# Performance work log

Measured on AMD Instinct MI355X. Metric: run time of the kernel, lower is better.

## Reference

```python
import jax, jax.numpy as jnp
import numpy as np

ND = 64       # dijetFeatures (channels)
NPAIR = 6     # six dijet slots


def _interleave(x, d):
    # x: [n, nd, 12] -> [n, nd, 6, 2]; d: [n, nd, 6] -> [n, nd, 6, 1]
    n, nd, _ = x.shape
    xr = x.reshape(n, nd, NPAIR, 2)
    z = jnp.concatenate([xr, d[..., None]], axis=-1)  # [n, nd, 6, 3]
    return z


def _conv_s3(z, W, b):
    # z: [n, in, 6, 3] grouped windows; W: [out, in, 3]; stride-3 k-3 conv == per-window contraction
    return jnp.einsum('bisk,oik->bos', z, W) + b[None, :, None]  # [n, out, 6]


def setup_inputs() -> dict:
    key = jax.random.key(0)
    ks = jax.random.split(key, 8)
    n = 65536
    inp = {
        'x': jax.random.normal(ks[0], (n, ND, 12), dtype=jnp.float32),
        'd': jax.random.normal(ks[1], (n, ND, NPAIR), dtype=jnp.float32),
        'W1': jax.random.normal(ks[2], (ND, ND, 3), dtype=jnp.float32) * 0.05,
        'b1': jax.random.normal(ks[3], (ND,), dtype=jnp.float32) * 0.05,
        'W2': jax.random.normal(ks[4], (ND, ND, 3), dtype=jnp.float32) * 0.05,
        'b2': jax.random.normal(ks[5], (ND,), dtype=jnp.float32) * 0.05,
        'W3': jax.random.normal(ks[6], (ND, ND, 3), dtype=jnp.float32) * 0.05,
        'b3': jax.random.normal(ks[7], (ND,), dtype=jnp.float32) * 0.05,
    }
    return inp


def reference(x, d, W1, b1, W2, b2, W3, b3):
    d1 = d
    d = jax.nn.relu(_conv_s3(_interleave(x, d), W1, b1))
    d = jax.nn.relu(_conv_s3(_interleave(x, d), W2, b2))
    d = _conv_s3(_interleave(x, d), W3, b3)
    return jax.nn.relu(d + d1)
```

## Files before the change

### kernel.cpp

```cpp
#include <hip/hip_runtime.h>

#define ND 64
#define NPAIR 6

typedef short bf16x8 __attribute__((ext_vector_type(8)));
typedef float floatx4 __attribute__((ext_vector_type(4)));

static constexpr int SPB  = 8;
static constexpr int ROWS = SPB * NPAIR;
static constexpr int ASTR = 200;

__device__ __forceinline__ unsigned short f2bf(float f) {
    unsigned u = __builtin_bit_cast(unsigned, f);
    u += 0x7FFFu + ((u >> 16) & 1u);
    return (unsigned short)(u >> 16);
}
__device__ __forceinline__ unsigned f2bf2(float lo, float hi) {
    return (unsigned)f2bf(lo) | ((unsigned)f2bf(hi) << 16);
}

__global__ void repack_w(const float* __restrict__ W1, const float* __restrict__ W2,
                         const float* __restrict__ W3, unsigned short* __restrict__ P) {
    int idx = blockIdx.x * 256 + threadIdx.x;
    if (idx >= 3 * 64 * 192) return;
    int j = idx % 192;
    int n = (idx / 192) % 64;
    int L = idx / (192 * 64);
    const float* W = (L == 0) ? W1 : (L == 1) ? W2 : W3;
    float v = (j < 128) ? W[n * 192 + (j >> 1) * 3 + (j & 1)]
                        : W[n * 192 + (j - 128) * 3 + 2];
    P[idx] = f2bf(v);
}

__global__ __launch_bounds__(256, 7) void dijet_main(
    const float* __restrict__ x, const float* __restrict__ d,
    const float* __restrict__ b1, const float* __restrict__ b2,
    const float* __restrict__ b3, const unsigned short* __restrict__ Wp,
    float* __restrict__ out)
{
    __shared__ __align__(16) unsigned short A[ROWS * ASTR];
    float* Ct = (float*)A;

    const int t  = threadIdx.x;
    const int b0 = blockIdx.x * SPB;

    float2 dres[6];
    {
        const float2* d2 = (const float2*)(d + (size_t)b0 * (ND * NPAIR));
        #pragma unroll
        for (int m = 0; m < 6; ++m) dres[m] = d2[m * 256 + t];
    }
    {
        const float4* x4 = (const float4*)(x + (size_t)b0 * (ND * 12));
        float4 v[6];
        #pragma unroll
        for (int m = 0; m < 6; ++m) v[m] = x4[m * 256 + t];
        unsigned* A32 = (unsigned*)A;
        #pragma unroll
        for (int m = 0; m < 6; ++m) {
            int idx = m * 256 + t;
            int b   = idx / 192;
            int rem = idx - b * 192;
            int i   = rem / 3;
            int c0  = (rem - i * 3) * 4;
            int row0 = b * 6 + (c0 >> 1);
            A32[row0 * (ASTR / 2) + i]       = f2bf2(v[m].x, v[m].y);
            A32[(row0 + 1) * (ASTR / 2) + i] = f2bf2(v[m].z, v[m].w);
        }
    }
    {
        #pragma unroll
        for (int m = 0; m < 6; ++m) {
            int idx = m * 256 + t;
            int e   = idx * 2;
            int b   = e / 384;
            int rem = e - b * 384;
            int i   = rem / 6;
            int s   = rem - i * 6;
            int row = b * 6 + s;
            A[row * ASTR + 128 + i]       = f2bf(dres[m].x);
            A[(row + 1) * ASTR + 128 + i] = f2bf(dres[m].y);
        }
    }
    __syncthreads();

    const int wave = t >> 6;
    const int lane = t & 63;
    const int l15  = lane & 15;
    const int quad = lane >> 4;
    const int nbase = wave * 16;

    #pragma unroll
    for (int L = 0; L < 3; ++L) {
        const float* bL = (L == 0) ? b1 : (L == 1) ? b2 : b3;
        const unsigned short* WL = Wp + L * (64 * 192);

        bf16x8 Bf[6];
        #pragma unroll
        for (int kk = 0; kk < 6; ++kk)
            Bf[kk] = *(const bf16x8*)(WL + (nbase + l15) * 192 + kk * 32 + quad * 8);
        float bias = bL[nbase + l15];

        floatx4 acc[3] = {};
        #pragma unroll
        for (int kk = 0; kk < 6; ++kk) {
            #pragma unroll
            for (int mt = 0; mt < 3; ++mt) {
                bf16x8 Af = *(const bf16x8*)(A + (mt * 16 + l15) * ASTR + kk * 32 + quad * 8);
                acc[mt] = __builtin_amdgcn_mfma_f32_16x16x32_bf16(Af, Bf[kk], acc[mt], 0, 0, 0);
            }
        }

        const int o = nbase + l15;
        if (L < 2) {
            __syncthreads();
            #pragma unroll
            for (int mt = 0; mt < 3; ++mt) {
                #pragma unroll
                for (int r = 0; r < 4; ++r) {
                    int row = mt * 16 + quad * 4 + r;
                    float v = acc[mt][r] + bias;
                    v = v > 0.f ? v : 0.f;
                    A[row * ASTR + 128 + o] = f2bf(v);
                }
            }
            __syncthreads();
        } else {
            __syncthreads();
            #pragma unroll
            for (int mt = 0; mt < 3; ++mt) {
                #pragma unroll
                for (int r = 0; r < 4; ++r) {
                    int row = mt * 16 + quad * 4 + r;
                    int bl  = row / 6;
                    int s   = row - bl * 6;
                    Ct[bl * (ND * NPAIR) + o * NPAIR + s] = acc[mt][r] + bias;
                }
            }
            __syncthreads();
            float2* out2 = (float2*)(out + (size_t)b0 * (ND * NPAIR));
            const float2* Ct2 = (const float2*)Ct;
            #pragma unroll
            for (int m = 0; m < 6; ++m) {
                int idx = m * 256 + t;
                float2 c = Ct2[idx];
                float2 r;
                r.x = c.x + dres[m].x; r.x = r.x > 0.f ? r.x : 0.f;
                r.y = c.y + dres[m].y; r.y = r.y > 0.f ? r.y : 0.f;
                out2[idx] = r;
            }
        }
    }
}

extern "C" void kernel_launch(void* const* d_in, const int* in_sizes, int n_in,
                              void* d_out, int out_size, void* d_ws, size_t ws_size,
                              hipStream_t stream)
{
    const float* x  = (const float*)d_in[0];
    const float* dd = (const float*)d_in[1];
    const float* W1 = (const float*)d_in[2];
    const float* b1 = (const float*)d_in[3];
    const float* W2 = (const float*)d_in[4];
    const float* b2 = (const float*)d_in[5];
    const float* W3 = (const float*)d_in[6];
    const float* b3 = (const float*)d_in[7];
    float* out = (float*)d_out;
    unsigned short* Wp = (unsigned short*)d_ws;

    int n = in_sizes[0] / (ND * 12);

    repack_w<<<144, 256, 0, stream>>>(W1, W2, W3, Wp);
    dijet_main<<<n / SPB, 256, 0, stream>>>(x, dd, b1, b2, b3, Wp, out);
}
```

Baseline: 392.5 us.

## Give each wave its own row tile and keep x fragments in registers

The work split changes from four waves each owning 16 output channels across all 48 rows to three waves each owning 16 rows across all 64 channels. The x part of the A operand is converted to bf16 straight into registers and reused across all three layers. Only the d/activation part goes through a smaller per-wave LDS region, so the block-wide barriers between layers go away and the layer outputs can be written as packed stores. The cost is that weight fragments are now read from global memory (L1/L2) inside the MFMA chain, x is loaded with strided float2 reads, and the block shrinks to 192 threads with a separate Ct buffer.

```diff
diff --git a/kernel.cpp b/kernel.cpp
--- a/kernel.cpp
+++ b/kernel.cpp
@@ -8,7 +8,7 @@
 
 static constexpr int SPB  = 8;
 static constexpr int ROWS = SPB * NPAIR;
-static constexpr int ASTR = 200;
+static constexpr int DSTR = 72;
 
 __device__ __forceinline__ unsigned short f2bf(float f) {
     unsigned u = __builtin_bit_cast(unsigned, f);
@@ -32,122 +32,115 @@
     P[idx] = f2bf(v);
 }
 
-__global__ __launch_bounds__(256, 7) void dijet_main(
+__global__ __launch_bounds__(192, 4) void dijet_main(
     const float* __restrict__ x, const float* __restrict__ d,
     const float* __restrict__ b1, const float* __restrict__ b2,
     const float* __restrict__ b3, const unsigned short* __restrict__ Wp,
     float* __restrict__ out)
 {
-    __shared__ __align__(16) unsigned short A[ROWS * ASTR];
-    float* Ct = (float*)A;
+    __shared__ __align__(16) unsigned short Adp[ROWS * DSTR];
+    __shared__ __align__(16) float Ct[SPB * ND * NPAIR];
 
-    const int t  = threadIdx.x;
-    const int b0 = blockIdx.x * SPB;
+    const int t    = threadIdx.x;
+    const int b0   = blockIdx.x * SPB;
+    const int wv   = t >> 6;
+    const int lane = t & 63;
+    const int l15  = lane & 15;
+    const int quad = lane >> 4;
 
-    float2 dres[6];
+    float2 dres[SPB];
     {
         const float2* d2 = (const float2*)(d + (size_t)b0 * (ND * NPAIR));
         #pragma unroll
-        for (int m = 0; m < 6; ++m) dres[m] = d2[m * 256 + t];
-    }
-    {
-        const float4* x4 = (const float4*)(x + (size_t)b0 * (ND * 12));
-        float4 v[6];
+        for (int m = 0; m < SPB; ++m) dres[m] = d2[m * 192 + t];
+        const int di  = t / 3;
+        const int dsl = 2 * (t - 3 * (t / 3));
         #pragma unroll
-        for (int m = 0; m < 6; ++m) v[m] = x4[m * 256 + t];
-        unsigned* A32 = (unsigned*)A;
-        #pragma unroll
-        for (int m = 0; m < 6; ++m) {
-            int idx = m * 256 + t;
-            int b   = idx / 192;
-            int rem = idx - b * 192;
-            int i   = rem / 3;
-            int c0  = (rem - i * 3) * 4;
-            int row0 = b * 6 + (c0 >> 1);
-            A32[row0 * (ASTR / 2) + i]       = f2bf2(v[m].x, v[m].y);
-            A32[(row0 + 1) * (ASTR / 2) + i] = f2bf2(v[m].z, v[m].w);
+        for (int m = 0; m < SPB; ++m) {
+            Adp[(m * 6 + dsl)     * DSTR + di] = f2bf(dres[m].x);
+            Adp[(m * 6 + dsl + 1) * DSTR + di] = f2bf(dres[m].y);
         }
     }
+
+    const int row = 16 * wv + l15;
+    const int bs  = row / 6;
+    const int ss  = row - 6 * bs;
+    bf16x8 Ax[4];
     {
+        const float* xb = x + (size_t)(b0 + bs) * (ND * 12) + 2 * ss;
         #pragma unroll
-        for (int m = 0; m < 6; ++m) {
-            int idx = m * 256 + t;
-            int e   = idx * 2;
-            int b   = e / 384;
-            int rem = e - b * 384;
-            int i   = rem / 6;
-            int s   = rem - i * 6;
-            int row = b * 6 + s;
-            A[row * ASTR + 128 + i]       = f2bf(dres[m].x);
-            A[(row + 1) * ASTR + 128 + i] = f2bf(dres[m].y);
+        for (int kk = 0; kk < 4; ++kk) {
+            union { bf16x8 h; unsigned u[4]; } tmp;
+            #pragma unroll
+            for (int w = 0; w < 4; ++w) {
+                const float2 v = *(const float2*)(xb + (kk * 16 + quad * 4 + w) * 12);
+                tmp.u[w] = f2bf2(v.x, v.y);
+            }
+            Ax[kk] = tmp.h;
         }
     }
     __syncthreads();
 
-    const int wave = t >> 6;
-    const int lane = t & 63;
-    const int l15  = lane & 15;
-    const int quad = lane >> 4;
-    const int nbase = wave * 16;
+    const unsigned short* Arow = Adp + (16 * wv + l15) * DSTR + quad * 8;
 
     #pragma unroll
     for (int L = 0; L < 3; ++L) {
         const float* bL = (L == 0) ? b1 : (L == 1) ? b2 : b3;
-        const unsigned short* WL = Wp + L * (64 * 192);
+        const unsigned short* WL = Wp + L * (64 * 192) + quad * 8;
 
-        bf16x8 Bf[6];
+        const bf16x8 Ad0 = *(const bf16x8*)(Arow);
+        const bf16x8 Ad1 = *(const bf16x8*)(Arow + 32);
+
+        float bias[4];
+        floatx4 acc[4];
         #pragma unroll
-        for (int kk = 0; kk < 6; ++kk)
-            Bf[kk] = *(const bf16x8*)(WL + (nbase + l15) * 192 + kk * 32 + quad * 8);
-        float bias = bL[nbase + l15];
-
-        floatx4 acc[3] = {};
-        #pragma unroll
-        for (int kk = 0; kk < 6; ++kk) {
-            #pragma unroll
-            for (int mt = 0; mt < 3; ++mt) {
-                bf16x8 Af = *(const bf16x8*)(A + (mt * 16 + l15) * ASTR + kk * 32 + quad * 8);
-                acc[mt] = __builtin_amdgcn_mfma_f32_16x16x32_bf16(Af, Bf[kk], acc[mt], 0, 0, 0);
-            }
+        for (int nt = 0; nt < 4; ++nt) {
+            const int ch = 4 * l15 + nt;
+            const unsigned short* wr = WL + ch * 192;
+            bias[nt] = bL[ch];
+            floatx4 a = {0.f, 0.f, 0.f, 0.f};
+            a = __builtin_amdgcn_mfma_f32_16x16x32_bf16(Ax[0], *(const bf16x8*)(wr),       a, 0, 0, 0);
+            a = __builtin_amdgcn_mfma_f32_16x16x32_bf16(Ax[1], *(const bf16x8*)(wr + 32),  a, 0, 0, 0);
+            a = __builtin_amdgcn_mfma_f32_16x16x32_bf16(Ax[2], *(const bf16x8*)(wr + 64),  a, 0, 0, 0);
+            a = __builtin_amdgcn_mfma_f32_16x16x32_bf16(Ax[3], *(const bf16x8*)(wr + 96),  a, 0, 0, 0);
+            a = __builtin_amdgcn_mfma_f32_16x16x32_bf16(Ad0,   *(const bf16x8*)(wr + 128), a, 0, 0, 0);
+            a = __builtin_amdgcn_mfma_f32_16x16x32_bf16(Ad1,   *(const bf16x8*)(wr + 160), a, 0, 0, 0);
+            acc[nt] = a;
         }
 
-        const int o = nbase + l15;
         if (L < 2) {
-            __syncthreads();
             #pragma unroll
-            for (int mt = 0; mt < 3; ++mt) {
+            for (int r = 0; r < 4; ++r) {
+                float v0 = acc[0][r] + bias[0]; v0 = v0 > 0.f ? v0 : 0.f;
+                float v1 = acc[1][r] + bias[1]; v1 = v1 > 0.f ? v1 : 0.f;
+                float v2 = acc[2][r] + bias[2]; v2 = v2 > 0.f ? v2 : 0.f;
+                float v3 = acc[3][r] + bias[3]; v3 = v3 > 0.f ? v3 : 0.f;
+                uint2 pk;
+                pk.x = f2bf2(v0, v1);
+                pk.y = f2bf2(v2, v3);
+                *(uint2*)(Adp + (16 * wv + quad * 4 + r) * DSTR + 4 * l15) = pk;
+            }
+        } else {
+            #pragma unroll
+            for (int nt = 0; nt < 4; ++nt) {
                 #pragma unroll
                 for (int r = 0; r < 4; ++r) {
-                    int row = mt * 16 + quad * 4 + r;
-                    float v = acc[mt][r] + bias;
-                    v = v > 0.f ? v : 0.f;
-                    A[row * ASTR + 128 + o] = f2bf(v);
-                }
-            }
-            __syncthreads();
-        } else {
-            __syncthreads();
-            #pragma unroll
-            for (int mt = 0; mt < 3; ++mt) {
-                #pragma unroll
-                for (int r = 0; r < 4; ++r) {
-                    int row = mt * 16 + quad * 4 + r;
-                    int bl  = row / 6;
-                    int s   = row - bl * 6;
-                    Ct[bl * (ND * NPAIR) + o * NPAIR + s] = acc[mt][r] + bias;
+                    const int rw = 16 * wv + quad * 4 + r;
+                    const int bl = rw / 6;
+                    const int s  = rw - 6 * bl;
+                    Ct[bl * (ND * NPAIR) + (4 * l15 + nt) * NPAIR + s] = acc[nt][r] + bias[nt];
                 }
             }
             __syncthreads();
             float2* out2 = (float2*)(out + (size_t)b0 * (ND * NPAIR));
             const float2* Ct2 = (const float2*)Ct;
             #pragma unroll
-            for (int m = 0; m < 6; ++m) {
-                int idx = m * 256 + t;
-                float2 c = Ct2[idx];
-                float2 r;
-                r.x = c.x + dres[m].x; r.x = r.x > 0.f ? r.x : 0.f;
-                r.y = c.y + dres[m].y; r.y = r.y > 0.f ? r.y : 0.f;
-                out2[idx] = r;
+            for (int m = 0; m < SPB; ++m) {
+                float2 c = Ct2[m * 192 + t];
+                float2 rv;
+                rv.x = c.x + dres[m].x; rv.x = rv.x > 0.f ? rv.x : 0.f;
+                rv.y = c.y + dres[m].y; rv.y = rv.y > 0.f ? rv.y : 0.f;
+                out2[m * 192 + t] = rv;
             }
         }
     }
@@ -171,5 +164,5 @@
     int n = in_sizes[0] / (ND * 12);
 
     repack_w<<<144, 256, 0, stream>>>(W1, W2, W3, Wp);
-    dijet_main<<<n / SPB, 256, 0, stream>>>(x, dd, b1, b2, b3, Wp, out);
+    dijet_main<<<n / SPB, 192, 0, stream>>>(x, dd, b1, b2, b3, Wp, out);
 }
```

Result: slower. 523.6 us (+33.4%).

## Split LDS into swizzled x buffer and double-buffered d tiles, drop a barrier

Applied to the files above, without the earlier changes.

Replaces the padded single A tile (stride 200) with an unpadded x tile plus two ping-pong d tiles, using XOR swizzles so the MFMA operand reads avoid bank conflicts without padding. Double-buffering the d activations removes one __syncthreads per layer, since the next layer's input is written to the other buffer. The launch-bounds occupancy hint drops from 7 to 6, and the LDS footprint changes slightly.

```diff
diff --git a/kernel.cpp b/kernel.cpp
--- a/kernel.cpp
+++ b/kernel.cpp
@@ -8,7 +8,6 @@
 
 static constexpr int SPB  = 8;
 static constexpr int ROWS = SPB * NPAIR;
-static constexpr int ASTR = 200;
 
 __device__ __forceinline__ unsigned short f2bf(float f) {
     unsigned u = __builtin_bit_cast(unsigned, f);
@@ -18,6 +17,9 @@
 __device__ __forceinline__ unsigned f2bf2(float lo, float hi) {
     return (unsigned)f2bf(lo) | ((unsigned)f2bf(hi) << 16);
 }
+
+__device__ __forceinline__ int swzAx(int row, int c) { return (c & 8) | ((c ^ row) & 7); }
+__device__ __forceinline__ int swzD (int row, int c) { return (c ^ row) & 7; }
 
 __global__ void repack_w(const float* __restrict__ W1, const float* __restrict__ W2,
                          const float* __restrict__ W3, unsigned short* __restrict__ P) {
@@ -32,14 +34,15 @@
     P[idx] = f2bf(v);
 }
 
-__global__ __launch_bounds__(256, 7) void dijet_main(
+__global__ __launch_bounds__(256, 6) void dijet_main(
     const float* __restrict__ x, const float* __restrict__ d,
     const float* __restrict__ b1, const float* __restrict__ b2,
     const float* __restrict__ b3, const unsigned short* __restrict__ Wp,
     float* __restrict__ out)
 {
-    __shared__ __align__(16) unsigned short A[ROWS * ASTR];
-    float* Ct = (float*)A;
+    __shared__ __align__(16) unsigned short Ax[ROWS * 128];
+    __shared__ __align__(16) unsigned short Dd[2][ROWS * 64];
+    float* Ct = (float*)Ax;
 
     const int t  = threadIdx.x;
     const int b0 = blockIdx.x * SPB;
@@ -49,26 +52,6 @@
         const float2* d2 = (const float2*)(d + (size_t)b0 * (ND * NPAIR));
         #pragma unroll
         for (int m = 0; m < 6; ++m) dres[m] = d2[m * 256 + t];
-    }
-    {
-        const float4* x4 = (const float4*)(x + (size_t)b0 * (ND * 12));
-        float4 v[6];
-        #pragma unroll
-        for (int m = 0; m < 6; ++m) v[m] = x4[m * 256 + t];
-        unsigned* A32 = (unsigned*)A;
-        #pragma unroll
-        for (int m = 0; m < 6; ++m) {
-            int idx = m * 256 + t;
-            int b   = idx / 192;
-            int rem = idx - b * 192;
-            int i   = rem / 3;
-            int c0  = (rem - i * 3) * 4;
-            int row0 = b * 6 + (c0 >> 1);
-            A32[row0 * (ASTR / 2) + i]       = f2bf2(v[m].x, v[m].y);
-            A32[(row0 + 1) * (ASTR / 2) + i] = f2bf2(v[m].z, v[m].w);
-        }
-    }
-    {
         #pragma unroll
         for (int m = 0; m < 6; ++m) {
             int idx = m * 256 + t;
@@ -78,8 +61,28 @@
             int i   = rem / 6;
             int s   = rem - i * 6;
             int row = b * 6 + s;
-            A[row * ASTR + 128 + i]       = f2bf(dres[m].x);
-            A[(row + 1) * ASTR + 128 + i] = f2bf(dres[m].y);
+            Dd[0][row * 64       + swzD(row, i >> 3) * 8     + (i & 7)] = f2bf(dres[m].x);
+            Dd[0][(row + 1) * 64 + swzD(row + 1, i >> 3) * 8 + (i & 7)] = f2bf(dres[m].y);
+        }
+    }
+    {
+        const float4* x4 = (const float4*)(x + (size_t)b0 * (ND * 12));
+        float4 v[6];
+        #pragma unroll
+        for (int m = 0; m < 6; ++m) v[m] = x4[m * 256 + t];
+        unsigned* Ax32 = (unsigned*)Ax;
+        #pragma unroll
+        for (int m = 0; m < 6; ++m) {
+            int idx = m * 256 + t;
+            int b   = idx / 192;
+            int rem = idx - b * 192;
+            int i   = rem / 3;
+            int c0  = (rem - i * 3) * 4;
+            int row0 = b * 6 + (c0 >> 1);
+            int row1 = row0 + 1;
+            int c    = i >> 2;
+            Ax32[row0 * 64 + swzAx(row0, c) * 4 + (i & 3)] = f2bf2(v[m].x, v[m].y);
+            Ax32[row1 * 64 + swzAx(row1, c) * 4 + (i & 3)] = f2bf2(v[m].z, v[m].w);
         }
     }
     __syncthreads();
@@ -90,6 +93,7 @@
     const int quad = lane >> 4;
     const int nbase = wave * 16;
 
+    int cur = 0;
     #pragma unroll
     for (int L = 0; L < 3; ++L) {
         const float* bL = (L == 0) ? b1 : (L == 1) ? b2 : b3;
@@ -103,17 +107,26 @@
 
         floatx4 acc[3] = {};
         #pragma unroll
-        for (int kk = 0; kk < 6; ++kk) {
+        for (int kk = 0; kk < 4; ++kk) {
             #pragma unroll
             for (int mt = 0; mt < 3; ++mt) {
-                bf16x8 Af = *(const bf16x8*)(A + (mt * 16 + l15) * ASTR + kk * 32 + quad * 8);
+                int row = mt * 16 + l15;
+                bf16x8 Af = *(const bf16x8*)(Ax + row * 128 + swzAx(row, kk * 4 + quad) * 8);
                 acc[mt] = __builtin_amdgcn_mfma_f32_16x16x32_bf16(Af, Bf[kk], acc[mt], 0, 0, 0);
+            }
+        }
+        #pragma unroll
+        for (int kz = 0; kz < 2; ++kz) {
+            #pragma unroll
+            for (int mt = 0; mt < 3; ++mt) {
+                int row = mt * 16 + l15;
+                bf16x8 Af = *(const bf16x8*)(Dd[cur] + row * 64 + swzD(row, kz * 4 + quad) * 8);
+                acc[mt] = __builtin_amdgcn_mfma_f32_16x16x32_bf16(Af, Bf[4 + kz], acc[mt], 0, 0, 0);
             }
         }
 
         const int o = nbase + l15;
         if (L < 2) {
-            __syncthreads();
             #pragma unroll
             for (int mt = 0; mt < 3; ++mt) {
                 #pragma unroll
@@ -121,10 +134,11 @@
                     int row = mt * 16 + quad * 4 + r;
                     float v = acc[mt][r] + bias;
                     v = v > 0.f ? v : 0.f;
-                    A[row * ASTR + 128 + o] = f2bf(v);
+                    Dd[cur ^ 1][row * 64 + swzD(row, o >> 3) * 8 + (o & 7)] = f2bf(v);
                 }
             }
             __syncthreads();
+            cur ^= 1;
         } else {
             __syncthreads();
             #pragma unroll
```

Result: no change. 393.8 us (+0.3%).
